# Optimization experiments

Measured on AMD Instinct MI355X. Metric: run time of the kernel, lower is better.

Reference implementation:

```python
import jax, jax.numpy as jnp
import numpy as np

N = 1048576      # obstacle points
E = 16           # polytope half-planes
HID = 32         # MLP hidden width
J = 10           # unrolled PDHG steps
TAU = 0.5
SIGMA = 0.5
RES = 0.5        # residual_scale for learned prox


def setup_inputs() -> dict:
    key = jax.random.key(0)
    ks = jax.random.split(key, 8)
    f32 = jnp.float32
    x = jax.random.normal(ks[0], (N, 2), dtype=f32) * 3.0
    # geometry buffers: regular 16-gon half-planes G mu <= h
    ang = np.arange(E) * (2.0 * np.pi / E)
    G = jnp.asarray(np.stack([np.cos(ang), np.sin(ang)], axis=1), dtype=f32)  # [E,2]
    h = jnp.ones((E, 1), dtype=f32)
    # encoder: Linear(2->HID), Linear(HID->HID)
    W1 = jax.random.normal(ks[1], (2, HID), dtype=f32) * 0.5
    b1 = jnp.zeros((HID,), dtype=f32)
    W2 = jax.random.normal(ks[2], (HID, HID), dtype=f32) * 0.2
    b2 = jnp.zeros((HID,), dtype=f32)
    # init_mu: Linear(HID->E); init_y: Linear(HID->2)
    Wmu = jax.random.normal(ks[3], (HID, E), dtype=f32) * 0.2
    bmu = jnp.zeros((E,), dtype=f32)
    Wy = jax.random.normal(ks[4], (HID, 2), dtype=f32) * 0.2
    by = jnp.zeros((2,), dtype=f32)
    # prox_head: Linear(2->HID) -> ReLU -> Linear(HID->E)
    Wp1 = jax.random.normal(ks[5], (2, HID), dtype=f32) * 0.5
    bp1 = jnp.zeros((HID,), dtype=f32)
    Wp2 = jax.random.normal(ks[6], (HID, E), dtype=f32) * 0.2
    bp2 = jnp.zeros((E,), dtype=f32)
    return dict(x=x, G=G, h=h, W1=W1, b1=b1, W2=W2, b2=b2,
                Wmu=Wmu, bmu=bmu, Wy=Wy, by=by,
                Wp1=Wp1, bp1=bp1, Wp2=Wp2, bp2=bp2)


def reference(x, G, h, W1, b1, W2, b2, Wmu, bmu, Wy, by, Wp1, bp1, Wp2, bp2):
    def project_mu(mu):
        # clamp_min(0), then scale rows so ||mu @ G||_2 <= 1
        mu = jnp.maximum(mu, 0.0)
        vn = jnp.linalg.norm(mu @ G, axis=1, keepdims=True)  # [N,1]
        return mu / jnp.maximum(vn, 1.0)

    feats = jax.nn.relu(x @ W1 + b1)
    feats = jax.nn.relu(feats @ W2 + b2)
    mu = jax.nn.relu(feats @ Wmu + bmu)          # [N,E]
    y = jnp.tanh(feats @ Wy + by)                # [N,2]
    a_row = x @ G.T - h.T                        # [N,E], constant across steps

    def step(carry, _):
        y, mu = carry
        # dual ascent + unit-ball projection on y
        y = y + SIGMA * (mu @ G)
        y = y / jnp.maximum(jnp.linalg.norm(y, axis=1, keepdims=True), 1.0)
        # primal update on mu
        mu = mu + TAU * (a_row - y @ G.T)
        # learned prox correction
        z = mu @ G                                # [N,2]
        delta = jax.nn.relu(z @ Wp1 + bp1) @ Wp2 + bp2
        mu = project_mu(mu + RES * delta)
        return (y, mu), None

    (y, mu), _ = jax.lax.scan(step, (y, mu), None, length=J)
    return project_mu(mu)
```

## Files before the change

### kernel.cpp

```cpp
#include <hip/hip_runtime.h>

#define E 16
#define HID 32
#define NSTEP 10
#define TAU 0.5f
#define SIGMA 0.5f
#define RES 0.5f
#define NT2 2
#define STRIDE 36

typedef __attribute__((ext_vector_type(8))) short bf16x8;
typedef __attribute__((ext_vector_type(16))) float f32x16;
typedef __attribute__((ext_vector_type(4))) unsigned int u32x4;

__device__ __forceinline__ f32x16 mfma32(bf16x8 a, bf16x8 b, f32x16 c) {
    return __builtin_amdgcn_mfma_f32_32x32x16_bf16(a, b, c, 0, 0, 0);
}
__device__ __forceinline__ unsigned int pk2(float lo, float hi) {
    unsigned int r;
    asm("v_cvt_pk_bf16_f32 %0, %1, %2" : "=v"(r) : "v"(lo), "v"(hi));
    return r;
}
__device__ __forceinline__ void split8(const float v[8], bf16x8& hi, bf16x8& lo) {
    u32x4 H, L;
#pragma unroll
    for (int j = 0; j < 4; ++j) {
        const unsigned int h = pk2(v[2 * j], v[2 * j + 1]);
        H[j] = h;
        const float h0 = __uint_as_float(h << 16);
        const float h1 = __uint_as_float(h & 0xffff0000u);
        L[j] = pk2(v[2 * j] - h0, v[2 * j + 1] - h1);
    }
    hi = __builtin_bit_cast(bf16x8, H);
    lo = __builtin_bit_cast(bf16x8, L);
}

__device__ __forceinline__ float fast_tanh(float v) {
    float e = __expf(2.0f * v);
    return 1.0f - __fdividef(2.0f, e + 1.0f);
}
__device__ __forceinline__ float inv_norm_clamped(float n2) {
    return fminf(__builtin_amdgcn_rsqf(n2), 1.0f);
}
__device__ __forceinline__ float bsum2(float x) { return x + __shfl_xor(x, 32); }

__global__ __attribute__((amdgpu_waves_per_eu(2, 3))) __launch_bounds__(256)
void pdhg_kernel(
    const float* __restrict__ xg,  const float* __restrict__ Gg,  const float* __restrict__ hg,
    const float* __restrict__ W1,  const float* __restrict__ b1,
    const float* __restrict__ W2,  const float* __restrict__ b2,
    const float* __restrict__ Wmu, const float* __restrict__ bmu,
    const float* __restrict__ Wy,  const float* __restrict__ by,
    const float* __restrict__ Wp1, const float* __restrict__ bp1,
    const float* __restrict__ Wp2, const float* __restrict__ bp2,
    float* __restrict__ out, int npts)
{
    __shared__ __align__(16) float sT[256 * STRIDE];
    const int tid = threadIdx.x;

    {
        const int pt = blockIdx.x * 256 + tid;
        const int ptc = min(pt, npts - 1);
        const float2 xv = reinterpret_cast<const float2*>(xg)[ptc];
        const float x0 = xv.x, x1 = xv.y;

        float g[HID];
        #pragma unroll
        for (int j = 0; j < HID; ++j) g[j] = b2[j];
        #pragma unroll
        for (int ci = 0; ci < 4; ++ci) {
            float fc[8];
            #pragma unroll
            for (int jj = 0; jj < 8; ++jj) {
                const int j = ci * 8 + jj;
                fc[jj] = fmaxf(fmaf(x0, W1[j], fmaf(x1, W1[HID + j], b1[j])), 0.0f);
            }
            #pragma unroll
            for (int ii = 0; ii < 8; ++ii) {
                const int i = ci * 8 + ii;
                #pragma unroll
                for (int j = 0; j < HID; ++j) g[j] = fmaf(fc[ii], W2[i * HID + j], g[j]);
            }
        }
        float* row = sT + tid * STRIDE;
        row[0] = x0; row[1] = x1;
        #pragma unroll
        for (int jq = 0; jq < 8; ++jq) {
            const int j = jq * 4;
            reinterpret_cast<float4*>(row + 4)[jq] = make_float4(
                fmaxf(g[j], 0.f), fmaxf(g[j + 1], 0.f),
                fmaxf(g[j + 2], 0.f), fmaxf(g[j + 3], 0.f));
        }
    }
    __syncthreads();

    const int lane = tid & 63;
    const int col  = lane & 31;
    const int kh   = lane >> 5;
    const bool colOK = col < E;
    const int colc = colOK ? col : 0;
    const int pbase = blockIdx.x * 256 + (tid >> 6) * 64;

    float gxr[8], gyr[8], thr8[8];
    f32x16 cinit;
    #pragma unroll
    for (int r = 0; r < 8; ++r) {
        const int e = (r & 3) + 8 * (r >> 2) + 4 * kh;
        gxr[r] = Gg[2 * e];
        gyr[r] = Gg[2 * e + 1];
        thr8[r] = TAU * hg[e];
        cinit[r] = bp2[e];
    }
    #pragma unroll
    for (int r = 8; r < 16; ++r) cinit[r] = 0.0f;

    float tg00, tg01, tg11;
    {
        float s00 = 0.f, s01 = 0.f, s11 = 0.f;
        #pragma unroll
        for (int r = 0; r < 8; ++r) {
            s00 = fmaf(gxr[r], gxr[r], s00);
            s01 = fmaf(gxr[r], gyr[r], s01);
            s11 = fmaf(gyr[r], gyr[r], s11);
        }
        tg00 = TAU * bsum2(s00);
        tg01 = TAU * bsum2(s01);
        tg11 = TAU * bsum2(s11);
    }

    bf16x8 wp2h[2], wp2l[2];
    #pragma unroll
    for (int w = 0; w < 2; ++w) {
        float wv[8];
        #pragma unroll
        for (int i = 0; i < 8; ++i) {
            const int k = w * 16 + kh * 8 + i;
            wv[i] = colOK ? Wp2[k * E + colc] : 0.0f;
        }
        split8(wv, wp2h[w], wp2l[w]);
    }
    float wp1a[16], wp1b[16], bp1r[16];
    #pragma unroll
    for (int w = 0; w < 2; ++w)
        #pragma unroll
        for (int i = 0; i < 8; ++i) {
            const int k = w * 16 + kh * 8 + i;
            wp1a[w * 8 + i] = Wp1[k];
            wp1b[w * 8 + i] = Wp1[HID + k];
            bp1r[w * 8 + i] = bp1[k];
        }

    float mu[NT2][8];
    float y0[NT2], y1[NT2], v0[NT2], v1[NT2], tc0[NT2], tc1[NT2];
    float tpx0[NT2], tpx1[NT2];

    {
        bf16x8 wmuh[2], wmul[2];
        #pragma unroll
        for (int w = 0; w < 2; ++w) {
            float wv[8];
            #pragma unroll
            for (int i = 0; i < 8; ++i) {
                const int k = w * 16 + kh * 8 + i;
                wv[i] = colOK ? Wmu[k * E + colc] : 0.0f;
            }
            split8(wv, wmuh[w], wmul[w]);
        }
        float wya[16], wyb[16];
        #pragma unroll
        for (int w = 0; w < 2; ++w)
            #pragma unroll
            for (int i = 0; i < 8; ++i) {
                const int k = w * 16 + kh * 8 + i;
                wya[w * 8 + i] = Wy[k * 2];
                wyb[w * 8 + i] = Wy[k * 2 + 1];
            }
        f32x16 cinitH;
        #pragma unroll
        for (int r = 0; r < 8; ++r)
            cinitH[r] = bmu[(r & 3) + 8 * (r >> 2) + 4 * kh];
        #pragma unroll
        for (int r = 8; r < 16; ++r) cinitH[r] = 0.0f;
        const float by0 = by[0], by1 = by[1];

        #pragma unroll
        for (int t = 0; t < NT2; ++t) {
            const float* prow = sT + (size_t)((tid >> 6) * 64 + t * 32 + col) * STRIDE;
            const float4* p4 = reinterpret_cast<const float4*>(prow);
            float gA[8], gB[8];
            {
                const float4 a0 = p4[1 + 2 * kh], a1 = p4[2 + 2 * kh];
                const float4 b0 = p4[5 + 2 * kh], b1v = p4[6 + 2 * kh];
                gA[0]=a0.x; gA[1]=a0.y; gA[2]=a0.z; gA[3]=a0.w;
                gA[4]=a1.x; gA[5]=a1.y; gA[6]=a1.z; gA[7]=a1.w;
                gB[0]=b0.x; gB[1]=b0.y; gB[2]=b0.z; gB[3]=b0.w;
                gB[4]=b1v.x; gB[5]=b1v.y; gB[6]=b1v.z; gB[7]=b1v.w;
            }
            const float px0 = prow[0], px1 = prow[1];
            float p0 = 0.f, p1 = 0.f;
            #pragma unroll
            for (int i = 0; i < 8; ++i) {
                p0 = fmaf(gA[i], wya[i], p0);      p1 = fmaf(gA[i], wyb[i], p1);
                p0 = fmaf(gB[i], wya[8 + i], p0);  p1 = fmaf(gB[i], wyb[8 + i], p1);
            }
            y0[t] = fast_tanh(by0 + bsum2(p0));
            y1[t] = fast_tanh(by1 + bsum2(p1));
            bf16x8 ghA, glA, ghB, glB;
            split8(gA, ghA, glA);
            split8(gB, ghB, glB);
            f32x16 d = mfma32(wmul[0], ghA, cinitH);
            d = mfma32(wmuh[0], glA, d);
            d = mfma32(wmuh[0], ghA, d);
            d = mfma32(wmul[1], ghB, d);
            d = mfma32(wmuh[1], glB, d);
            d = mfma32(wmuh[1], ghB, d);
            float q0 = 0.f, q1 = 0.f, r0 = 0.f, r1 = 0.f;
            #pragma unroll
            for (int r = 0; r < 8; ++r) {
                const float m = fmaxf(d[r], 0.0f);
                mu[t][r] = m;
                const float tae = fmaf(TAU, fmaf(px0, gxr[r], px1 * gyr[r]), -thr8[r]);
                q0 = fmaf(tae, gxr[r], q0);
                q1 = fmaf(tae, gyr[r], q1);
                r0 = fmaf(m, gxr[r], r0);
                r1 = fmaf(m, gyr[r], r1);
            }
            tc0[t] = bsum2(q0); tc1[t] = bsum2(q1);
            v0[t]  = bsum2(r0); v1[t]  = bsum2(r1);
            tpx0[t] = TAU * px0; tpx1[t] = TAU * px1;
        }
    }

    #pragma unroll 1
    for (int s = 0; s < NSTEP; ++s) {
        #pragma unroll
        for (int t = 0; t < NT2; ++t) {
            float a0 = fmaf(SIGMA, v0[t], y0[t]);
            float a1 = fmaf(SIGMA, v1[t], y1[t]);
            const float sc = inv_norm_clamped(fmaf(a0, a0, a1 * a1));
            a0 *= sc; a1 *= sc;
            y0[t] = a0; y1[t] = a1;
            const float z0 = fmaf(-tg00, a0, fmaf(-tg01, a1, v0[t] + tc0[t]));
            const float z1 = fmaf(-tg01, a0, fmaf(-tg11, a1, v1[t] + tc1[t]));
            const float u0 = fmaf(-TAU, a0, tpx0[t]);
            const float u1 = fmaf(-TAU, a1, tpx1[t]);
            #pragma unroll
            for (int r = 0; r < 8; ++r)
                mu[t][r] = fmaf(u1, gyr[r], fmaf(u0, gxr[r], mu[t][r] - thr8[r]));

            f32x16 d;
            {
                float hk[8];
                #pragma unroll
                for (int i = 0; i < 8; ++i)
                    hk[i] = fmaxf(fmaf(z0, wp1a[i], fmaf(z1, wp1b[i], bp1r[i])), 0.0f);
                bf16x8 bh, bl;
                split8(hk, bh, bl);
                d = mfma32(wp2l[0], bh, cinit);
                d = mfma32(wp2h[0], bl, d);
                d = mfma32(wp2h[0], bh, d);
            }
            {
                float hk[8];
                #pragma unroll
                for (int i = 0; i < 8; ++i)
                    hk[i] = fmaxf(fmaf(z0, wp1a[8 + i], fmaf(z1, wp1b[8 + i], bp1r[8 + i])), 0.0f);
                bf16x8 bh, bl;
                split8(hk, bh, bl);
                d = mfma32(wp2l[1], bh, d);
                d = mfma32(wp2h[1], bl, d);
                d = mfma32(wp2h[1], bh, d);
            }

            float p0 = 0.f, p1 = 0.f;
            #pragma unroll
            for (int r = 0; r < 8; ++r) {
                const float m = fmaxf(fmaf(RES, d[r], mu[t][r]), 0.0f);
                mu[t][r] = m;
                p0 = fmaf(m, gxr[r], p0);
                p1 = fmaf(m, gyr[r], p1);
            }
            p0 = bsum2(p0); p1 = bsum2(p1);
            const float sp = inv_norm_clamped(fmaf(p0, p0, p1 * p1));
            #pragma unroll
            for (int r = 0; r < 8; ++r) mu[t][r] *= sp;
            v0[t] = sp * p0;
            v1[t] = sp * p1;
        }
    }

    #pragma unroll
    for (int t = 0; t < NT2; ++t) {
        const int q = pbase + t * 32 + col;
        if (q < npts) {
            float* o = out + (size_t)q * E;
            *reinterpret_cast<float4*>(o + 4 * kh) =
                make_float4(mu[t][0], mu[t][1], mu[t][2], mu[t][3]);
            *reinterpret_cast<float4*>(o + 8 + 4 * kh) =
                make_float4(mu[t][4], mu[t][5], mu[t][6], mu[t][7]);
        }
    }
}

extern "C" void kernel_launch(void* const* d_in, const int* in_sizes, int n_in,
                              void* d_out, int out_size, void* d_ws, size_t ws_size,
                              hipStream_t stream) {
    const float* x   = (const float*)d_in[0];
    const float* G   = (const float*)d_in[1];
    const float* h   = (const float*)d_in[2];
    const float* W1  = (const float*)d_in[3];
    const float* b1  = (const float*)d_in[4];
    const float* W2  = (const float*)d_in[5];
    const float* b2  = (const float*)d_in[6];
    const float* Wmu = (const float*)d_in[7];
    const float* bmu = (const float*)d_in[8];
    const float* Wy  = (const float*)d_in[9];
    const float* by  = (const float*)d_in[10];
    const float* Wp1 = (const float*)d_in[11];
    const float* bp1 = (const float*)d_in[12];
    const float* Wp2 = (const float*)d_in[13];
    const float* bp2 = (const float*)d_in[14];

    const int npts = in_sizes[0] / 2;
    const int block = 256;
    const int grid = (npts + block - 1) / block;

    pdhg_kernel<<<grid, block, 0, stream>>>(x, G, h, W1, b1, W2, b2, Wmu, bmu,
                                            Wy, by, Wp1, bp1, Wp2, bp2,
                                            (float*)d_out, npts);
}
```

Before: 248.3 us.

## Process two points per thread with 128-thread blocks and four MFMA tiles per wave

Halves the block size to 128 threads while keeping 256 points per block. Each thread now runs the encoder MLP for two points, so every W1/W2 weight load is shared across two FMAs. Each wave handles four 32-point MFMA tiles instead of two, which amortizes the per-wave setup of weights and constants. The cost is more register pressure and fewer waves in flight, which may cut latency hiding.

```diff
diff --git a/kernel.cpp b/kernel.cpp
--- a/kernel.cpp
+++ b/kernel.cpp
@@ -6,7 +6,7 @@
 #define TAU 0.5f
 #define SIGMA 0.5f
 #define RES 0.5f
-#define NT2 2
+#define NT2 4
 #define STRIDE 36
 
 typedef __attribute__((ext_vector_type(8))) short bf16x8;
@@ -44,7 +44,7 @@
 }
 __device__ __forceinline__ float bsum2(float x) { return x + __shfl_xor(x, 32); }
 
-__global__ __attribute__((amdgpu_waves_per_eu(2, 3))) __launch_bounds__(256)
+__global__ __attribute__((amdgpu_waves_per_eu(2, 3))) __launch_bounds__(128)
 void pdhg_kernel(
     const float* __restrict__ xg,  const float* __restrict__ Gg,  const float* __restrict__ hg,
     const float* __restrict__ W1,  const float* __restrict__ b1,
@@ -59,47 +59,65 @@
     const int tid = threadIdx.x;
 
     {
-        const int pt = blockIdx.x * 256 + tid;
-        const int ptc = min(pt, npts - 1);
-        const float2 xv = reinterpret_cast<const float2*>(xg)[ptc];
-        const float x0 = xv.x, x1 = xv.y;
-
-        float g[HID];
-        #pragma unroll
-        for (int j = 0; j < HID; ++j) g[j] = b2[j];
+        const int base = blockIdx.x * 256;
+        const int pA = min(base + tid,        npts - 1);
+        const int pB = min(base + tid + 128,  npts - 1);
+        const float2 xa = reinterpret_cast<const float2*>(xg)[pA];
+        const float2 xb = reinterpret_cast<const float2*>(xg)[pB];
+        const float x0[2] = { xa.x, xb.x };
+        const float x1[2] = { xa.y, xb.y };
+
+        float g[2][HID];
+        #pragma unroll
+        for (int j = 0; j < HID; ++j) {
+            const float bb = b2[j];
+            g[0][j] = bb; g[1][j] = bb;
+        }
         #pragma unroll
         for (int ci = 0; ci < 4; ++ci) {
-            float fc[8];
+            float fc[2][8];
             #pragma unroll
             for (int jj = 0; jj < 8; ++jj) {
                 const int j = ci * 8 + jj;
-                fc[jj] = fmaxf(fmaf(x0, W1[j], fmaf(x1, W1[HID + j], b1[j])), 0.0f);
+                const float w0 = W1[j], w1 = W1[HID + j], bb = b1[j];
+                #pragma unroll
+                for (int p = 0; p < 2; ++p)
+                    fc[p][jj] = fmaxf(fmaf(x0[p], w0, fmaf(x1[p], w1, bb)), 0.0f);
             }
             #pragma unroll
             for (int ii = 0; ii < 8; ++ii) {
                 const int i = ci * 8 + ii;
                 #pragma unroll
-                for (int j = 0; j < HID; ++j) g[j] = fmaf(fc[ii], W2[i * HID + j], g[j]);
-            }
-        }
-        float* row = sT + tid * STRIDE;
-        row[0] = x0; row[1] = x1;
-        #pragma unroll
-        for (int jq = 0; jq < 8; ++jq) {
-            const int j = jq * 4;
-            reinterpret_cast<float4*>(row + 4)[jq] = make_float4(
-                fmaxf(g[j], 0.f), fmaxf(g[j + 1], 0.f),
-                fmaxf(g[j + 2], 0.f), fmaxf(g[j + 3], 0.f));
+                for (int j = 0; j < HID; ++j) {
+                    const float w = W2[i * HID + j];
+                    g[0][j] = fmaf(fc[0][ii], w, g[0][j]);
+                    g[1][j] = fmaf(fc[1][ii], w, g[1][j]);
+                }
+            }
+        }
+        #pragma unroll
+        for (int p = 0; p < 2; ++p) {
+            float* row = sT + (size_t)(tid + p * 128) * STRIDE;
+            row[0] = x0[p]; row[1] = x1[p];
+            #pragma unroll
+            for (int jq = 0; jq < 8; ++jq) {
+                const int j = jq * 4;
+                reinterpret_cast<float4*>(row + 4)[jq] = make_float4(
+                    fmaxf(g[p][j], 0.f), fmaxf(g[p][j + 1], 0.f),
+                    fmaxf(g[p][j + 2], 0.f), fmaxf(g[p][j + 3], 0.f));
+            }
         }
     }
     __syncthreads();
 
     const int lane = tid & 63;
+    const int wv   = tid >> 6;
     const int col  = lane & 31;
     const int kh   = lane >> 5;
     const bool colOK = col < E;
     const int colc = colOK ? col : 0;
-    const int pbase = blockIdx.x * 256 + (tid >> 6) * 64;
+    const int lbase = wv * 128;
+    const int pbase = blockIdx.x * 256 + lbase;
 
     float gxr[8], gyr[8], thr8[8];
     f32x16 cinit;
@@ -131,13 +149,13 @@
     bf16x8 wp2h[2], wp2l[2];
     #pragma unroll
     for (int w = 0; w < 2; ++w) {
-        float wv[8];
+        float wvv[8];
         #pragma unroll
         for (int i = 0; i < 8; ++i) {
             const int k = w * 16 + kh * 8 + i;
-            wv[i] = colOK ? Wp2[k * E + colc] : 0.0f;
-        }
-        split8(wv, wp2h[w], wp2l[w]);
+            wvv[i] = colOK ? Wp2[k * E + colc] : 0.0f;
+        }
+        split8(wvv, wp2h[w], wp2l[w]);
     }
     float wp1a[16], wp1b[16], bp1r[16];
     #pragma unroll
@@ -158,13 +176,13 @@
         bf16x8 wmuh[2], wmul[2];
         #pragma unroll
         for (int w = 0; w < 2; ++w) {
-            float wv[8];
+            float wvv[8];
             #pragma unroll
             for (int i = 0; i < 8; ++i) {
                 const int k = w * 16 + kh * 8 + i;
-                wv[i] = colOK ? Wmu[k * E + colc] : 0.0f;
-            }
-            split8(wv, wmuh[w], wmul[w]);
+                wvv[i] = colOK ? Wmu[k * E + colc] : 0.0f;
+            }
+            split8(wvv, wmuh[w], wmul[w]);
         }
         float wya[16], wyb[16];
         #pragma unroll
@@ -185,7 +203,7 @@
 
         #pragma unroll
         for (int t = 0; t < NT2; ++t) {
-            const float* prow = sT + (size_t)((tid >> 6) * 64 + t * 32 + col) * STRIDE;
+            const float* prow = sT + (size_t)(lbase + t * 32 + col) * STRIDE;
             const float4* p4 = reinterpret_cast<const float4*>(prow);
             float gA[8], gB[8];
             {
@@ -322,8 +340,8 @@
     const float* bp2 = (const float*)d_in[14];
 
     const int npts = in_sizes[0] / 2;
-    const int block = 256;
-    const int grid = (npts + block - 1) / block;
+    const int block = 128;
+    const int grid = (npts + 255) / 256;
 
     pdhg_kernel<<<grid, block, 0, stream>>>(x, G, h, W1, b1, W2, b2, Wmu, bmu,
                                             Wy, by, Wp1, bp1, Wp2, bp2,
```

Measured after the change: 279.5 us. 12.6% more time.
